# Kernel optimization log

Measured on AMD Instinct MI355X. Metric: run time of the kernel, lower is better.

## Reference

```python
import jax, jax.numpy as jnp
import numpy as np

DIM = 256
NUM_HEADS = 8


def setup_inputs() -> dict:
    key = jax.random.key(0)
    ks = jax.random.split(key, 5)
    x = jax.random.normal(ks[0], (32, DIM, 56, 56), dtype=jnp.float32)
    # Conv2d(dim, 2*dim, k=1, groups=2): weight [2*dim, dim//2, 1, 1]
    qk_w = jax.random.normal(ks[1], (2 * DIM, DIM // 2, 1, 1), dtype=jnp.float32) * (DIM // 2) ** -0.5
    qk_b = jax.random.normal(ks[2], (2 * DIM,), dtype=jnp.float32) * 0.02
    # Conv2d(dim, dim, k=3, pad=1, groups=dim): weight [dim, 1, 3, 3]
    pe_w = jax.random.normal(ks[3], (DIM, 1, 3, 3), dtype=jnp.float32) * (1.0 / 3.0)
    pe_b = jax.random.normal(ks[4], (DIM,), dtype=jnp.float32) * 0.02
    return {"x": x, "qk_w": qk_w, "qk_b": qk_b, "pe_w": pe_w, "pe_b": pe_b}


def _conv(x, w, padding, groups):
    return jax.lax.conv_general_dilated(
        x, w, window_strides=(1, 1), padding=padding,
        feature_group_count=groups,
        dimension_numbers=("NCHW", "OIHW", "NCHW"))


def reference(x, qk_w, qk_b, pe_w, pe_b):
    b, c, h, w = x.shape
    H, hd = NUM_HEADS, c // NUM_HEADS
    n = h * w
    s = n ** (-0.5)

    # grouped 1x1 conv -> elu + 1 feature map
    qk = _conv(x, qk_w, "VALID", groups=2) + qk_b[None, :, None, None]
    qk = jax.nn.elu(qk) + 1.0                       # [b, 2c, h, w]
    qk = qk.reshape(b, 2, H, hd, n)
    q, k = qk[:, 0], qk[:, 1]                       # [b, H, hd, n]
    v = x.reshape(b, H, hd, n)                      # [b, H, hd, n]

    # kv = (k*s) @ (v^T * s)  -> [b, H, hd, hd]
    kv = jnp.einsum("bhdn,bhen->bhde", k * s, v * s)
    # numerator: q^T @ kv -> [b, H, n, hd]
    num = jnp.einsum("bhdn,bhde->bhne", q, kv)
    # denominator: q^T @ mean_n(k) -> [b, H, n]
    den = jnp.einsum("bhdn,bhd->bhn", q, k.mean(axis=-1))
    out = num / (den[..., None] + 1e-6)             # [b, H, n, hd]

    out = out.transpose(0, 1, 3, 2).reshape(b, c, h, w)
    pe = _conv(x, pe_w, [(1, 1), (1, 1)], groups=c) + pe_b[None, :, None, None]
    return out + pe
```

## Files before the change

### kernel.cpp

```cpp
#include <hip/hip_runtime.h>
#include <cmath>

#define NCH   256
#define NPIX  3136
#define NB    32
#define SEV   7
#define INV_N (1.0f / 3136.0f)

typedef __attribute__((ext_vector_type(8)))  short bf16x8;
typedef __attribute__((ext_vector_type(4)))  float f32x4;
typedef __attribute__((ext_vector_type(16))) float f32x16;

#define KV7_F  (SEV * NB * 8 * 1024)
#define KM7_F  (SEV * NB * 256)
#define KVF_F  (NB * 8 * 1024)
#define KMF_F  (NB * 256)
#define KM7_OFF (KV7_F)
#define KVF_OFF (KM7_OFF + KM7_F)
#define KMF_OFF (KVF_OFF + KVF_F)
#define WF_OFF  (KMF_OFF + KMF_F)

__device__ __forceinline__ ushort f2bf(float f) {
  unsigned u = __float_as_uint(f);
  u += 0x7FFFu + ((u >> 16) & 1u);
  return (ushort)(u >> 16);
}
__device__ __forceinline__ float bf2f(ushort h) {
  return __uint_as_float(((unsigned)h) << 16);
}

__global__ void wfrag_kernel(const float* __restrict__ qk_w, ushort* __restrict__ Wf) {
  const int tid = blockIdx.x * 512 + threadIdx.x;
  const int lane = tid & 63;
  const int ks = (tid >> 6) & 3;
  const int mt = (tid >> 8) & 15;
  const int hl = (tid >> 12) & 1;
  const int side = (tid >> 13) & 1;
  const int ch = mt * 16 + (lane & 15);
  const int oc = side * 256 + ch;
  ushort v[8];
#pragma unroll
  for (int j = 0; j < 8; ++j) {
    const int k = ks * 32 + (lane >> 4) * 8 + j;
    const float w = qk_w[(size_t)oc * 128 + k];
    const ushort hi = f2bf(w);
    v[j] = (hl == 0) ? hi : f2bf(w - bf2f(hi));
  }
  *(uint4*)(Wf + (size_t)tid * 8) = *(const uint4*)v;
}

__global__ __launch_bounds__(512)
void pe_kernel(const float* __restrict__ x, const float* __restrict__ pe_w,
               const float* __restrict__ pe_b, float* __restrict__ out) {
  const int b = blockIdx.y;
  const int t = threadIdx.x;
  const int w = t >> 6;
  const int l = t & 63;
  const int c = blockIdx.x * 8 + w;

  const bool act = (l < 56);
  const int c4 = act ? (l % 14) : 0;
  const int rq = act ? (l / 14) : 0;
  const int col = c4 * 4;
  const bool hasL = act && (c4 > 0);
  const bool hasR = (c4 < 13);
  const int lnL = (l + 63) & 63, lnR = (l + 1) & 63;

  const float* xc = x + ((size_t)(b * NCH + c)) * NPIX;
  float* oc = out + ((size_t)(b * NCH + c)) * NPIX;

  float pw[9];
#pragma unroll
  for (int i = 0; i < 9; ++i) pw[i] = pe_w[c * 9 + i];
  const float pb = pe_b[c];
  const float4 Z = {0.f, 0.f, 0.f, 0.f};

#pragma unroll
  for (int sb = 0; sb < 4; ++sb) {
    const int bi0 = sb * 4 + rq;
    const bool bact = act && (bi0 < 14);
    const int bi = (bi0 < 14) ? bi0 : 13;
    const int r0 = bi * 4;

    float4 m = (r0 > 0) ? *(const float4*)(xc + (r0 - 1) * 56 + col) : Z;
    float4 cc = *(const float4*)(xc + r0 * 56 + col);
    float mLw = __shfl(m.w, lnL), mRx = __shfl(m.x, lnR);
    float cLw = __shfl(cc.w, lnL), cRx = __shfl(cc.x, lnR);

#pragma unroll
    for (int k = 0; k < 4; ++k) {
      const int rp = r0 + k + 1;
      const float4 p = (rp < 56) ? *(const float4*)(xc + rp * 56 + col) : Z;
      const float pLw = __shfl(p.w, lnL);
      const float pRx = __shfl(p.x, lnR);

      const float Lm = hasL ? mLw : 0.f;
      const float Lc = hasL ? cLw : 0.f;
      const float Lp = hasL ? pLw : 0.f;
      const float Rm = hasR ? mRx : 0.f;
      const float Rc = hasR ? cRx : 0.f;
      const float Rp = hasR ? pRx : 0.f;

      float4 res;
      res.x = pb + pw[0] * Lm  + pw[1] * m.x + pw[2] * m.y
                 + pw[3] * Lc  + pw[4] * cc.x + pw[5] * cc.y
                 + pw[6] * Lp  + pw[7] * p.x + pw[8] * p.y;
      res.y = pb + pw[0] * m.x + pw[1] * m.y + pw[2] * m.z
                 + pw[3] * cc.x + pw[4] * cc.y + pw[5] * cc.z
                 + pw[6] * p.x + pw[7] * p.y + pw[8] * p.z;
      res.z = pb + pw[0] * m.y + pw[1] * m.z + pw[2] * m.w
                 + pw[3] * cc.y + pw[4] * cc.z + pw[5] * cc.w
                 + pw[6] * p.y + pw[7] * p.z + pw[8] * p.w;
      res.w = pb + pw[0] * m.z + pw[1] * m.w + pw[2] * Rm
                 + pw[3] * cc.z + pw[4] * cc.w + pw[5] * Rc
                 + pw[6] * p.z + pw[7] * p.w + pw[8] * Rp;

      if (bact) *(float4*)(oc + (r0 + k) * 56 + col) = res;

      m = cc; mLw = cLw; mRx = cRx;
      cc = p; cLw = pLw; cRx = pRx;
    }
  }
}

__global__ __launch_bounds__(512, 4)
void kv_kernel(const float* __restrict__ x, const ushort* __restrict__ Wf,
               const float* __restrict__ qk_b, float* __restrict__ kv7,
               float* __restrict__ km7) {
  const int bid = blockIdx.x;
  const int hd = (bid >= 224) ? 1 : 0;
  const int rem = bid - hd * 224;
  const int sev = rem >> 5, b = rem & 31;
  const int t = threadIdx.x;
  const int w = t >> 6, l = t & 63;
  const int q = l >> 4, r15 = l & 15;
  const int e = l & 31, q5 = l >> 5;
  const int h_l = w & 3, ph = w >> 2;
  const int mt = w;

  __shared__ __align__(16) ushort Xb[64][152];
  __shared__ __align__(16) ushort KVs[2 * 128 * 88];
  ushort (*Kst)[88] = (ushort(*)[88])KVs;
  ushort (*Vst)[88] = (ushort(*)[88])(KVs + 128 * 88);

  bf16x8 wf[4][2];
#pragma unroll
  for (int ks = 0; ks < 4; ++ks)
#pragma unroll
    for (int hl = 0; hl < 2; ++hl) {
      const size_t off =
          (size_t)(((((2 + hl) * 16 + (hd * 8 + mt)) * 4 + ks) * 64 + l)) * 8;
      wf[ks][hl] = *(const bf16x8*)(Wf + off);
    }

  float bias[4];
#pragma unroll
  for (int r = 0; r < 4; ++r)
    bias[r] = qk_b[256 + hd * 128 + mt * 16 + q * 4 + r];

  f32x16 kvacc;
#pragma unroll
  for (int i = 0; i < 16; ++i) kvacc[i] = 0.f;
  float kmacc[4] = {0.f, 0.f, 0.f, 0.f};

  const float* xk = x + ((size_t)(b * NCH) + 128) * NPIX + sev * 448;
  const float* xv = x + ((size_t)(b * NCH)) * NPIX + sev * 448;

  for (int st = 0; st < SEV; ++st) {
    const int p0 = st * 64;
    __syncthreads();

#pragma unroll
    for (int rr = 0; rr < 4; ++rr) {
      const int id = t + 512 * rr;
      const int cc = id >> 4;
      const int pf = id & 15;
      const float4 v = *(const float4*)(xk + (size_t)cc * NPIX + p0 + pf * 4);
      const ushort b0 = f2bf(v.x), b1 = f2bf(v.y), b2 = f2bf(v.z), b3 = f2bf(v.w);
      Xb[pf * 4 + 0][cc] = b0;
      Xb[pf * 4 + 1][cc] = b1;
      Xb[pf * 4 + 2][cc] = b2;
      Xb[pf * 4 + 3][cc] = b3;
      if (hd == 1) {
        const uint2 pk = {(uint)b0 | ((uint)b1 << 16), (uint)b2 | ((uint)b3 << 16)};
        *(uint2*)&Vst[cc][pf * 4] = pk;
      }
    }
    if (hd == 0) {
#pragma unroll
      for (int rr = 0; rr < 4; ++rr) {
        const int id = t + 512 * rr;
        const int cc = id >> 4;
        const int pf = id & 15;
        const float4 v = *(const float4*)(xv + (size_t)cc * NPIX + p0 + pf * 4);
        const uint2 pk = {(uint)f2bf(v.x) | ((uint)f2bf(v.y) << 16),
                          (uint)f2bf(v.z) | ((uint)f2bf(v.w) << 16)};
        *(uint2*)&Vst[cc][pf * 4] = pk;
      }
    }
    __syncthreads();

    f32x4 acc[4];
#pragma unroll
    for (int nt = 0; nt < 4; ++nt)
#pragma unroll
      for (int r = 0; r < 4; ++r) acc[nt][r] = 0.f;
#pragma unroll
    for (int ks = 0; ks < 4; ++ks) {
      bf16x8 xbf[4];
#pragma unroll
      for (int nt = 0; nt < 4; ++nt)
        xbf[nt] = *(const bf16x8*)&Xb[nt * 16 + r15][ks * 32 + q * 8];
#pragma unroll
      for (int nt = 0; nt < 4; ++nt) {
        acc[nt] = __builtin_amdgcn_mfma_f32_16x16x32_bf16(wf[ks][0], xbf[nt], acc[nt], 0, 0, 0);
        acc[nt] = __builtin_amdgcn_mfma_f32_16x16x32_bf16(wf[ks][1], xbf[nt], acc[nt], 0, 0, 0);
      }
    }

#pragma unroll
    for (int nt = 0; nt < 4; ++nt) {
#pragma unroll
      for (int r = 0; r < 4; ++r) {
        float v = acc[nt][r] + bias[r];
        v = (v > 0.f) ? (v + 1.f) : __expf(v);
        kmacc[r] += v;
        Kst[mt * 16 + q * 4 + r][nt * 16 + r15] = f2bf(v);
      }
    }
    __syncthreads();

#pragma unroll
    for (int ks2 = 0; ks2 < 2; ++ks2) {
      const int kp = ph * 32 + ks2 * 16 + q5 * 8;
      const bf16x8 ak = *(const bf16x8*)&Kst[h_l * 32 + e][kp];
      const bf16x8 bv = *(const bf16x8*)&Vst[h_l * 32 + e][kp];
      kvacc = __builtin_amdgcn_mfma_f32_32x32x16_bf16(ak, bv, kvacc, 0, 0, 0);
    }
  }

  __syncthreads();
  float* red = (float*)KVs;
#pragma unroll
  for (int reg = 0; reg < 16; ++reg) {
    const int row = (reg & 3) + 8 * (reg >> 2) + 4 * q5;
    red[w * 1024 + row * 32 + e] = kvacc[reg];
  }
  __syncthreads();
#pragma unroll
  for (int i = 0; i < 8; ++i) {
    const int idx = t + 512 * i;
    const int hl2 = idx >> 10;
    const int el = idx & 1023;
    const float s = red[hl2 * 1024 + el] + red[(hl2 + 4) * 1024 + el];
    kv7[(((size_t)sev * NB + b) * 8 + hd * 4 + hl2) * 1024 + el] = s;
  }
#pragma unroll
  for (int r = 0; r < 4; ++r) {
    float s = kmacc[r];
    s += __shfl_xor(s, 1);
    s += __shfl_xor(s, 2);
    s += __shfl_xor(s, 4);
    s += __shfl_xor(s, 8);
    if (r15 == 0)
      km7[((size_t)sev * NB + b) * 256 + hd * 128 + mt * 16 + q * 4 + r] = s;
  }
}

__global__ void red_kernel(const float* __restrict__ kv7, const float* __restrict__ km7,
                           float* __restrict__ kvF, float* __restrict__ kmF) {
  const int b = blockIdx.x;
  const int t = threadIdx.x;
  for (int i = t; i < 8192; i += 256) {
    float s = 0.f;
#pragma unroll
    for (int sv = 0; sv < SEV; ++sv)
      s += kv7[(size_t)(sv * NB + b) * 8192 + i];
    kvF[(size_t)b * 8192 + i] = s * INV_N;
  }
  {
    float s = 0.f;
#pragma unroll
    for (int sv = 0; sv < SEV; ++sv)
      s += km7[(size_t)(sv * NB + b) * 256 + t];
    kmF[b * 256 + t] = s * INV_N;
  }
}

__global__ __launch_bounds__(512, 4)
void out_kernel(const float* __restrict__ x, const ushort* __restrict__ Wf,
                const float* __restrict__ qk_b, const float* __restrict__ kvF,
                const float* __restrict__ kmF, float* __restrict__ out) {
  const int bid = blockIdx.x;
  const int hd = (bid >= 224) ? 1 : 0;
  const int rem = bid - hd * 224;
  const int b = rem & 31, sev = rem >> 5;
  const int t = threadIdx.x;
  const int w = t >> 6, l = t & 63;
  const int q = l >> 4, r15 = l & 15;
  const int mt = w;
  const int h_l = w & 3, eh = w >> 2;

  __shared__ ushort Xb[64][136];
  __shared__ ushort QT[64][136];
  __shared__ float denP[8][64];

  bf16x8 wf[4][2];
#pragma unroll
  for (int ks = 0; ks < 4; ++ks)
#pragma unroll
    for (int hl = 0; hl < 2; ++hl) {
      const size_t off =
          (size_t)((((hl * 16 + (hd * 8 + mt)) * 4 + ks) * 64 + l)) * 8;
      wf[ks][hl] = *(const bf16x8*)(Wf + off);
    }

  float bias[4], kmw[4];
#pragma unroll
  for (int r = 0; r < 4; ++r) {
    const int c = hd * 128 + mt * 16 + q * 4 + r;
    bias[r] = qk_b[c];
    kmw[r] = kmF[b * 256 + c];
  }

  bf16x8 bkv;
  {
    const int hg = hd * 4 + h_l;
#pragma unroll
    for (int j = 0; j < 8; ++j)
      bkv[j] = (short)f2bf(
          kvF[(size_t)b * 8192 + hg * 1024 + (q * 8 + j) * 32 + eh * 16 + r15]);
  }

  const float* xq = x + (size_t)(b * NCH) * NPIX + sev * 448;

  for (int st = 0; st < SEV; ++st) {
    const int pos0 = st * 64;
#pragma unroll
    for (int rr = 0; rr < 4; ++rr) {
      const int id = t + 512 * rr;
      const int ch = id >> 4;
      const int p4 = (id & 15) * 4;
      const float4 v = *(const float4*)(xq + (size_t)ch * NPIX + pos0 + p4);
      Xb[p4 + 0][ch] = f2bf(v.x);
      Xb[p4 + 1][ch] = f2bf(v.y);
      Xb[p4 + 2][ch] = f2bf(v.z);
      Xb[p4 + 3][ch] = f2bf(v.w);
    }
    __syncthreads();

    f32x4 acc[4];
#pragma unroll
    for (int nt = 0; nt < 4; ++nt)
#pragma unroll
      for (int r = 0; r < 4; ++r) acc[nt][r] = 0.f;
#pragma unroll
    for (int ks = 0; ks < 4; ++ks) {
      bf16x8 xbf[4];
#pragma unroll
      for (int nt = 0; nt < 4; ++nt)
        xbf[nt] = *(const bf16x8*)&Xb[nt * 16 + r15][ks * 32 + q * 8];
#pragma unroll
      for (int nt = 0; nt < 4; ++nt) {
        acc[nt] = __builtin_amdgcn_mfma_f32_16x16x32_bf16(wf[ks][0], xbf[nt], acc[nt], 0, 0, 0);
        acc[nt] = __builtin_amdgcn_mfma_f32_16x16x32_bf16(wf[ks][1], xbf[nt], acc[nt], 0, 0, 0);
      }
    }

#pragma unroll
    for (int nt = 0; nt < 4; ++nt) {
      ushort pk[4];
      float dsum = 0.f;
#pragma unroll
      for (int r = 0; r < 4; ++r) {
        float v = acc[nt][r] + bias[r];
        v = (v > 0.f) ? (v + 1.f) : __expf(v);
        pk[r] = f2bf(v);
        dsum += v * kmw[r];
      }
      *(uint2*)&QT[nt * 16 + r15][mt * 16 + q * 4] = *(const uint2*)pk;
      dsum += __shfl_xor(dsum, 16);
      dsum += __shfl_xor(dsum, 32);
      if (q == 0) denP[mt][nt * 16 + r15] = dsum;
    }
    __syncthreads();

#pragma unroll
    for (int pt = 0; pt < 4; ++pt) {
      const bf16x8 aq = *(const bf16x8*)&QT[pt * 16 + r15][h_l * 32 + q * 8];
      f32x4 z;
      z[0] = z[1] = z[2] = z[3] = 0.f;
      const f32x4 n0 = __builtin_amdgcn_mfma_f32_16x16x32_bf16(aq, bkv, z, 0, 0, 0);
      float rdn[4];
#pragma unroll
      for (int r = 0; r < 4; ++r) {
        const int pl = pt * 16 + q * 4 + r;
        rdn[r] = 1.0f / (denP[2 * h_l][pl] + denP[2 * h_l + 1][pl] + 1e-6f);
      }
      const int posg = sev * 448 + pos0 + pt * 16 + q * 4;
      const int c = hd * 128 + h_l * 32 + eh * 16 + r15;
      float* op = out + ((size_t)(b * NCH + c)) * NPIX + posg;
      float4 prev = *(const float4*)op;
      prev.x += n0[0] * rdn[0];
      prev.y += n0[1] * rdn[1];
      prev.z += n0[2] * rdn[2];
      prev.w += n0[3] * rdn[3];
      *(float4*)op = prev;
    }
    __syncthreads();
  }
}

extern "C" void kernel_launch(void* const* d_in, const int* in_sizes, int n_in,
                              void* d_out, int out_size, void* d_ws,
                              size_t ws_size, hipStream_t stream) {
  const float* x    = (const float*)d_in[0];
  const float* qk_w = (const float*)d_in[1];
  const float* qk_b = (const float*)d_in[2];
  const float* pe_w = (const float*)d_in[3];
  const float* pe_b = (const float*)d_in[4];
  float* out = (float*)d_out;

  float* wsf = (float*)d_ws;
  float* kv7 = wsf;
  float* km7 = wsf + KM7_OFF;
  float* kvF = wsf + KVF_OFF;
  float* kmF = wsf + KMF_OFF;
  ushort* Wf = (ushort*)(wsf + WF_OFF);

  dim3 gp(32, NB);
  pe_kernel<<<gp, 512, 0, stream>>>(x, pe_w, pe_b, out);
  wfrag_kernel<<<32, 512, 0, stream>>>(qk_w, Wf);
  kv_kernel<<<448, 512, 0, stream>>>(x, Wf, qk_b, kv7, km7);
  red_kernel<<<NB, 256, 0, stream>>>(kv7, km7, kvF, kmF);
  out_kernel<<<448, 512, 0, stream>>>(x, Wf, qk_b, kvF, kmF, out);
}
```

Baseline: 142.0 us.

## Fuse depthwise positional conv into kv kernel via interleaved block roles

```diff
diff --git a/kernel.cpp b/kernel.cpp
--- a/kernel.cpp
+++ b/kernel.cpp
@@ -49,221 +49,223 @@
   *(uint4*)(Wf + (size_t)tid * 8) = *(const uint4*)v;
 }
 
-__global__ __launch_bounds__(512)
-void pe_kernel(const float* __restrict__ x, const float* __restrict__ pe_w,
-               const float* __restrict__ pe_b, float* __restrict__ out) {
-  const int b = blockIdx.y;
-  const int t = threadIdx.x;
-  const int w = t >> 6;
-  const int l = t & 63;
-  const int c = blockIdx.x * 8 + w;
-
-  const bool act = (l < 56);
-  const int c4 = act ? (l % 14) : 0;
-  const int rq = act ? (l / 14) : 0;
-  const int col = c4 * 4;
-  const bool hasL = act && (c4 > 0);
-  const bool hasR = (c4 < 13);
-  const int lnL = (l + 63) & 63, lnR = (l + 1) & 63;
-
-  const float* xc = x + ((size_t)(b * NCH + c)) * NPIX;
-  float* oc = out + ((size_t)(b * NCH + c)) * NPIX;
-
-  float pw[9];
-#pragma unroll
-  for (int i = 0; i < 9; ++i) pw[i] = pe_w[c * 9 + i];
-  const float pb = pe_b[c];
-  const float4 Z = {0.f, 0.f, 0.f, 0.f};
-
-#pragma unroll
-  for (int sb = 0; sb < 4; ++sb) {
-    const int bi0 = sb * 4 + rq;
-    const bool bact = act && (bi0 < 14);
-    const int bi = (bi0 < 14) ? bi0 : 13;
-    const int r0 = bi * 4;
-
-    float4 m = (r0 > 0) ? *(const float4*)(xc + (r0 - 1) * 56 + col) : Z;
-    float4 cc = *(const float4*)(xc + r0 * 56 + col);
-    float mLw = __shfl(m.w, lnL), mRx = __shfl(m.x, lnR);
-    float cLw = __shfl(cc.w, lnL), cRx = __shfl(cc.x, lnR);
-
-#pragma unroll
-    for (int k = 0; k < 4; ++k) {
-      const int rp = r0 + k + 1;
-      const float4 p = (rp < 56) ? *(const float4*)(xc + rp * 56 + col) : Z;
-      const float pLw = __shfl(p.w, lnL);
-      const float pRx = __shfl(p.x, lnR);
-
-      const float Lm = hasL ? mLw : 0.f;
-      const float Lc = hasL ? cLw : 0.f;
-      const float Lp = hasL ? pLw : 0.f;
-      const float Rm = hasR ? mRx : 0.f;
-      const float Rc = hasR ? cRx : 0.f;
-      const float Rp = hasR ? pRx : 0.f;
-
-      float4 res;
-      res.x = pb + pw[0] * Lm  + pw[1] * m.x + pw[2] * m.y
-                 + pw[3] * Lc  + pw[4] * cc.x + pw[5] * cc.y
-                 + pw[6] * Lp  + pw[7] * p.x + pw[8] * p.y;
-      res.y = pb + pw[0] * m.x + pw[1] * m.y + pw[2] * m.z
-                 + pw[3] * cc.x + pw[4] * cc.y + pw[5] * cc.z
-                 + pw[6] * p.x + pw[7] * p.y + pw[8] * p.z;
-      res.z = pb + pw[0] * m.y + pw[1] * m.z + pw[2] * m.w
-                 + pw[3] * cc.y + pw[4] * cc.z + pw[5] * cc.w
-                 + pw[6] * p.y + pw[7] * p.z + pw[8] * p.w;
-      res.w = pb + pw[0] * m.z + pw[1] * m.w + pw[2] * Rm
-                 + pw[3] * cc.z + pw[4] * cc.w + pw[5] * Rc
-                 + pw[6] * p.z + pw[7] * p.w + pw[8] * Rp;
-
-      if (bact) *(float4*)(oc + (r0 + k) * 56 + col) = res;
-
-      m = cc; mLw = cLw; mRx = cRx;
-      cc = p; cLw = pLw; cRx = pRx;
-    }
-  }
-}
-
 __global__ __launch_bounds__(512, 4)
-void kv_kernel(const float* __restrict__ x, const ushort* __restrict__ Wf,
-               const float* __restrict__ qk_b, float* __restrict__ kv7,
-               float* __restrict__ km7) {
-  const int bid = blockIdx.x;
-  const int hd = (bid >= 224) ? 1 : 0;
-  const int rem = bid - hd * 224;
-  const int sev = rem >> 5, b = rem & 31;
+void kvpe_kernel(const float* __restrict__ x, const ushort* __restrict__ Wf,
+                 const float* __restrict__ qk_b, const float* __restrict__ pe_w,
+                 const float* __restrict__ pe_b, float* __restrict__ kv7,
+                 float* __restrict__ km7, float* __restrict__ out) {
+  const int g = blockIdx.x;
+  const int r23 = g % 23;
+  const int grp = g / 23;
   const int t = threadIdx.x;
   const int w = t >> 6, l = t & 63;
-  const int q = l >> 4, r15 = l & 15;
-  const int e = l & 31, q5 = l >> 5;
-  const int h_l = w & 3, ph = w >> 2;
-  const int mt = w;
 
   __shared__ __align__(16) ushort Xb[64][152];
   __shared__ __align__(16) ushort KVs[2 * 128 * 88];
-  ushort (*Kst)[88] = (ushort(*)[88])KVs;
-  ushort (*Vst)[88] = (ushort(*)[88])(KVs + 128 * 88);
-
-  bf16x8 wf[4][2];
-#pragma unroll
-  for (int ks = 0; ks < 4; ++ks)
-#pragma unroll
-    for (int hl = 0; hl < 2; ++hl) {
-      const size_t off =
-          (size_t)(((((2 + hl) * 16 + (hd * 8 + mt)) * 4 + ks) * 64 + l)) * 8;
-      wf[ks][hl] = *(const bf16x8*)(Wf + off);
-    }
-
-  float bias[4];
-#pragma unroll
-  for (int r = 0; r < 4; ++r)
-    bias[r] = qk_b[256 + hd * 128 + mt * 16 + q * 4 + r];
-
-  f32x16 kvacc;
-#pragma unroll
-  for (int i = 0; i < 16; ++i) kvacc[i] = 0.f;
-  float kmacc[4] = {0.f, 0.f, 0.f, 0.f};
-
-  const float* xk = x + ((size_t)(b * NCH) + 128) * NPIX + sev * 448;
-  const float* xv = x + ((size_t)(b * NCH)) * NPIX + sev * 448;
-
-  for (int st = 0; st < SEV; ++st) {
-    const int p0 = st * 64;
-    __syncthreads();
-
-#pragma unroll
-    for (int rr = 0; rr < 4; ++rr) {
-      const int id = t + 512 * rr;
-      const int cc = id >> 4;
-      const int pf = id & 15;
-      const float4 v = *(const float4*)(xk + (size_t)cc * NPIX + p0 + pf * 4);
-      const ushort b0 = f2bf(v.x), b1 = f2bf(v.y), b2 = f2bf(v.z), b3 = f2bf(v.w);
-      Xb[pf * 4 + 0][cc] = b0;
-      Xb[pf * 4 + 1][cc] = b1;
-      Xb[pf * 4 + 2][cc] = b2;
-      Xb[pf * 4 + 3][cc] = b3;
-      if (hd == 1) {
-        const uint2 pk = {(uint)b0 | ((uint)b1 << 16), (uint)b2 | ((uint)b3 << 16)};
-        *(uint2*)&Vst[cc][pf * 4] = pk;
-      }
-    }
-    if (hd == 0) {
+
+  if (r23 < 7) {
+    const int kvid = grp * 7 + r23;
+    const int hd = (kvid >= 224) ? 1 : 0;
+    const int rem = kvid - hd * 224;
+    const int sev = rem >> 5, b = rem & 31;
+    const int q = l >> 4, r15 = l & 15;
+    const int e = l & 31, q5 = l >> 5;
+    const int h_l = w & 3, ph = w >> 2;
+    const int mt = w;
+
+    ushort (*Kst)[88] = (ushort(*)[88])KVs;
+    ushort (*Vst)[88] = (ushort(*)[88])(KVs + 128 * 88);
+
+    bf16x8 wf[4][2];
+#pragma unroll
+    for (int ks = 0; ks < 4; ++ks)
+#pragma unroll
+      for (int hl = 0; hl < 2; ++hl) {
+        const size_t off =
+            (size_t)(((((2 + hl) * 16 + (hd * 8 + mt)) * 4 + ks) * 64 + l)) * 8;
+        wf[ks][hl] = *(const bf16x8*)(Wf + off);
+      }
+
+    float bias[4];
+#pragma unroll
+    for (int r = 0; r < 4; ++r)
+      bias[r] = qk_b[256 + hd * 128 + mt * 16 + q * 4 + r];
+
+    f32x16 kvacc;
+#pragma unroll
+    for (int i = 0; i < 16; ++i) kvacc[i] = 0.f;
+    float kmacc[4] = {0.f, 0.f, 0.f, 0.f};
+
+    const float* xk = x + ((size_t)(b * NCH) + 128) * NPIX + sev * 448;
+    const float* xv = x + ((size_t)(b * NCH)) * NPIX + sev * 448;
+
+    for (int st = 0; st < SEV; ++st) {
+      const int p0 = st * 64;
+      __syncthreads();
+
 #pragma unroll
       for (int rr = 0; rr < 4; ++rr) {
         const int id = t + 512 * rr;
         const int cc = id >> 4;
         const int pf = id & 15;
-        const float4 v = *(const float4*)(xv + (size_t)cc * NPIX + p0 + pf * 4);
-        const uint2 pk = {(uint)f2bf(v.x) | ((uint)f2bf(v.y) << 16),
-                          (uint)f2bf(v.z) | ((uint)f2bf(v.w) << 16)};
-        *(uint2*)&Vst[cc][pf * 4] = pk;
-      }
-    }
+        const float4 v = *(const float4*)(xk + (size_t)cc * NPIX + p0 + pf * 4);
+        const ushort b0 = f2bf(v.x), b1 = f2bf(v.y), b2 = f2bf(v.z), b3 = f2bf(v.w);
+        Xb[pf * 4 + 0][cc] = b0;
+        Xb[pf * 4 + 1][cc] = b1;
+        Xb[pf * 4 + 2][cc] = b2;
+        Xb[pf * 4 + 3][cc] = b3;
+        if (hd == 1) {
+          const uint2 pk = {(uint)b0 | ((uint)b1 << 16), (uint)b2 | ((uint)b3 << 16)};
+          *(uint2*)&Vst[cc][pf * 4] = pk;
+        }
+      }
+      if (hd == 0) {
+#pragma unroll
+        for (int rr = 0; rr < 4; ++rr) {
+          const int id = t + 512 * rr;
+          const int cc = id >> 4;
+          const int pf = id & 15;
+          const float4 v = *(const float4*)(xv + (size_t)cc * NPIX + p0 + pf * 4);
+          const uint2 pk = {(uint)f2bf(v.x) | ((uint)f2bf(v.y) << 16),
+                            (uint)f2bf(v.z) | ((uint)f2bf(v.w) << 16)};
+          *(uint2*)&Vst[cc][pf * 4] = pk;
+        }
+      }
+      __syncthreads();
+
+      f32x4 acc[4];
+#pragma unroll
+      for (int nt = 0; nt < 4; ++nt)
+#pragma unroll
+        for (int r = 0; r < 4; ++r) acc[nt][r] = 0.f;
+#pragma unroll
+      for (int ks = 0; ks < 4; ++ks) {
+        bf16x8 xbf[4];
+#pragma unroll
+        for (int nt = 0; nt < 4; ++nt)
+          xbf[nt] = *(const bf16x8*)&Xb[nt * 16 + r15][ks * 32 + q * 8];
+#pragma unroll
+        for (int nt = 0; nt < 4; ++nt) {
+          acc[nt] = __builtin_amdgcn_mfma_f32_16x16x32_bf16(wf[ks][0], xbf[nt], acc[nt], 0, 0, 0);
+          acc[nt] = __builtin_amdgcn_mfma_f32_16x16x32_bf16(wf[ks][1], xbf[nt], acc[nt], 0, 0, 0);
+        }
+      }
+
+#pragma unroll
+      for (int nt = 0; nt < 4; ++nt) {
+#pragma unroll
+        for (int r = 0; r < 4; ++r) {
+          float v = acc[nt][r] + bias[r];
+          v = (v > 0.f) ? (v + 1.f) : __expf(v);
+          kmacc[r] += v;
+          Kst[mt * 16 + q * 4 + r][nt * 16 + r15] = f2bf(v);
+        }
+      }
+      __syncthreads();
+
+#pragma unroll
+      for (int ks2 = 0; ks2 < 2; ++ks2) {
+        const int kp = ph * 32 + ks2 * 16 + q5 * 8;
+        const bf16x8 ak = *(const bf16x8*)&Kst[h_l * 32 + e][kp];
+        const bf16x8 bv = *(const bf16x8*)&Vst[h_l * 32 + e][kp];
+        kvacc = __builtin_amdgcn_mfma_f32_32x32x16_bf16(ak, bv, kvacc, 0, 0, 0);
+      }
+    }
+
     __syncthreads();
-
-    f32x4 acc[4];
-#pragma unroll
-    for (int nt = 0; nt < 4; ++nt)
-#pragma unroll
-      for (int r = 0; r < 4; ++r) acc[nt][r] = 0.f;
-#pragma unroll
-    for (int ks = 0; ks < 4; ++ks) {
-      bf16x8 xbf[4];
-#pragma unroll
-      for (int nt = 0; nt < 4; ++nt)
-        xbf[nt] = *(const bf16x8*)&Xb[nt * 16 + r15][ks * 32 + q * 8];
-#pragma unroll
-      for (int nt = 0; nt < 4; ++nt) {
-        acc[nt] = __builtin_amdgcn_mfma_f32_16x16x32_bf16(wf[ks][0], xbf[nt], acc[nt], 0, 0, 0);
-        acc[nt] = __builtin_amdgcn_mfma_f32_16x16x32_bf16(wf[ks][1], xbf[nt], acc[nt], 0, 0, 0);
-      }
-    }
-
-#pragma unroll
-    for (int nt = 0; nt < 4; ++nt) {
-#pragma unroll
-      for (int r = 0; r < 4; ++r) {
-        float v = acc[nt][r] + bias[r];
-        v = (v > 0.f) ? (v + 1.f) : __expf(v);
-        kmacc[r] += v;
-        Kst[mt * 16 + q * 4 + r][nt * 16 + r15] = f2bf(v);
-      }
+    float* red = (float*)KVs;
+#pragma unroll
+    for (int reg = 0; reg < 16; ++reg) {
+      const int row = (reg & 3) + 8 * (reg >> 2) + 4 * q5;
+      red[w * 1024 + row * 32 + e] = kvacc[reg];
     }
     __syncthreads();
-
-#pragma unroll
-    for (int ks2 = 0; ks2 < 2; ++ks2) {
-      const int kp = ph * 32 + ks2 * 16 + q5 * 8;
-      const bf16x8 ak = *(const bf16x8*)&Kst[h_l * 32 + e][kp];
-      const bf16x8 bv = *(const bf16x8*)&Vst[h_l * 32 + e][kp];
-      kvacc = __builtin_amdgcn_mfma_f32_32x32x16_bf16(ak, bv, kvacc, 0, 0, 0);
-    }
-  }
-
-  __syncthreads();
-  float* red = (float*)KVs;
-#pragma unroll
-  for (int reg = 0; reg < 16; ++reg) {
-    const int row = (reg & 3) + 8 * (reg >> 2) + 4 * q5;
-    red[w * 1024 + row * 32 + e] = kvacc[reg];
-  }
-  __syncthreads();
-#pragma unroll
-  for (int i = 0; i < 8; ++i) {
-    const int idx = t + 512 * i;
-    const int hl2 = idx >> 10;
-    const int el = idx & 1023;
-    const float s = red[hl2 * 1024 + el] + red[(hl2 + 4) * 1024 + el];
-    kv7[(((size_t)sev * NB + b) * 8 + hd * 4 + hl2) * 1024 + el] = s;
-  }
-#pragma unroll
-  for (int r = 0; r < 4; ++r) {
-    float s = kmacc[r];
-    s += __shfl_xor(s, 1);
-    s += __shfl_xor(s, 2);
-    s += __shfl_xor(s, 4);
-    s += __shfl_xor(s, 8);
-    if (r15 == 0)
-      km7[((size_t)sev * NB + b) * 256 + hd * 128 + mt * 16 + q * 4 + r] = s;
+#pragma unroll
+    for (int i = 0; i < 8; ++i) {
+      const int idx = t + 512 * i;
+      const int hl2 = idx >> 10;
+      const int el = idx & 1023;
+      const float s = red[hl2 * 1024 + el] + red[(hl2 + 4) * 1024 + el];
+      kv7[(((size_t)sev * NB + b) * 8 + hd * 4 + hl2) * 1024 + el] = s;
+    }
+#pragma unroll
+    for (int r = 0; r < 4; ++r) {
+      float s = kmacc[r];
+      s += __shfl_xor(s, 1);
+      s += __shfl_xor(s, 2);
+      s += __shfl_xor(s, 4);
+      s += __shfl_xor(s, 8);
+      if (r15 == 0)
+        km7[((size_t)sev * NB + b) * 256 + hd * 128 + mt * 16 + q * 4 + r] = s;
+    }
+  } else {
+    const int pid = grp * 16 + (r23 - 7);
+    const int b = pid >> 5;
+    const int c = (pid & 31) * 8 + w;
+
+    const bool act = (l < 56);
+    const int c4 = act ? (l % 14) : 0;
+    const int rq = act ? (l / 14) : 0;
+    const int col = c4 * 4;
+    const bool hasL = act && (c4 > 0);
+    const bool hasR = (c4 < 13);
+    const int lnL = (l + 63) & 63, lnR = (l + 1) & 63;
+
+    const float* xc = x + ((size_t)(b * NCH + c)) * NPIX;
+    float* oc = out + ((size_t)(b * NCH + c)) * NPIX;
+
+    float pw[9];
+#pragma unroll
+    for (int i = 0; i < 9; ++i) pw[i] = pe_w[c * 9 + i];
+    const float pb = pe_b[c];
+    const float4 Z = {0.f, 0.f, 0.f, 0.f};
+
+#pragma unroll
+    for (int sb = 0; sb < 4; ++sb) {
+      const int bi0 = sb * 4 + rq;
+      const bool bact = act && (bi0 < 14);
+      const int bi = (bi0 < 14) ? bi0 : 13;
+      const int r0 = bi * 4;
+
+      float4 m = (r0 > 0) ? *(const float4*)(xc + (r0 - 1) * 56 + col) : Z;
+      float4 cc = *(const float4*)(xc + r0 * 56 + col);
+      float mLw = __shfl(m.w, lnL), mRx = __shfl(m.x, lnR);
+      float cLw = __shfl(cc.w, lnL), cRx = __shfl(cc.x, lnR);
+
+#pragma unroll
+      for (int k = 0; k < 4; ++k) {
+        const int rp = r0 + k + 1;
+        const float4 p = (rp < 56) ? *(const float4*)(xc + rp * 56 + col) : Z;
+        const float pLw = __shfl(p.w, lnL);
+        const float pRx = __shfl(p.x, lnR);
+
+        const float Lm = hasL ? mLw : 0.f;
+        const float Lc = hasL ? cLw : 0.f;
+        const float Lp = hasL ? pLw : 0.f;
+        const float Rm = hasR ? mRx : 0.f;
+        const float Rc = hasR ? cRx : 0.f;
+        const float Rp = hasR ? pRx : 0.f;
+
+        float4 res;
+        res.x = pb + pw[0] * Lm  + pw[1] * m.x + pw[2] * m.y
+                   + pw[3] * Lc  + pw[4] * cc.x + pw[5] * cc.y
+                   + pw[6] * Lp  + pw[7] * p.x + pw[8] * p.y;
+        res.y = pb + pw[0] * m.x + pw[1] * m.y + pw[2] * m.z
+                   + pw[3] * cc.x + pw[4] * cc.y + pw[5] * cc.z
+                   + pw[6] * p.x + pw[7] * p.y + pw[8] * p.z;
+        res.z = pb + pw[0] * m.y + pw[1] * m.z + pw[2] * m.w
+                   + pw[3] * cc.y + pw[4] * cc.z + pw[5] * cc.w
+                   + pw[6] * p.y + pw[7] * p.z + pw[8] * p.w;
+        res.w = pb + pw[0] * m.z + pw[1] * m.w + pw[2] * Rm
+                   + pw[3] * cc.z + pw[4] * cc.w + pw[5] * Rc
+                   + pw[6] * p.z + pw[7] * p.w + pw[8] * Rp;
+
+        if (bact) *(float4*)(oc + (r0 + k) * 56 + col) = res;
+
+        m = cc; mLw = cLw; mRx = cRx;
+        cc = p; cLw = pLw; cRx = pRx;
+      }
+    }
   }
 }
 
@@ -428,10 +430,8 @@
   float* kmF = wsf + KMF_OFF;
   ushort* Wf = (ushort*)(wsf + WF_OFF);
 
-  dim3 gp(32, NB);
-  pe_kernel<<<gp, 512, 0, stream>>>(x, pe_w, pe_b, out);
   wfrag_kernel<<<32, 512, 0, stream>>>(qk_w, Wf);
-  kv_kernel<<<448, 512, 0, stream>>>(x, Wf, qk_b, kv7, km7);
+  kvpe_kernel<<<1472, 512, 0, stream>>>(x, Wf, qk_b, pe_w, pe_b, kv7, km7, out);
   red_kernel<<<NB, 256, 0, stream>>>(kv7, km7, kvF, kmF);
   out_kernel<<<448, 512, 0, stream>>>(x, Wf, qk_b, kvF, kmF, out);
 }
```

Result: slower. 147.0 us (+3.5%).
